# Kernel optimization log

Hardware: AMD Instinct MI355X
Metric: run time of the kernel (lower is better)

## Reference

```python
import jax, jax.numpy as jnp
import numpy as np

B, H, S, D = 2, 12, 2048, 64


def setup_inputs() -> dict:
    key = jax.random.key(0)
    kq, kk, kv = jax.random.split(key, 3)
    q = jax.random.normal(kq, (B, H, S, D), dtype=jnp.float32)
    k = jax.random.normal(kk, (B, H, S, D), dtype=jnp.float32)
    v = jax.random.normal(kv, (B, H, S, D), dtype=jnp.float32)
    # causal mask: True = attend (keep), lower triangle
    mask = jnp.tril(jnp.ones((S, S), dtype=bool))
    return {"q": q, "k": k, "v": v, "mask": mask}


def reference(q, k, v, mask):
    dim = q.shape[-1]
    # [B,H,S,S] scores
    scores = jnp.einsum("bhqd,bhkd->bhqk", q, k) / jnp.sqrt(jnp.asarray(dim, q.dtype))
    # dynamic mask-direction logic from the original module:
    # if the mask is denser in the strict upper triangle, True means "mask out";
    # otherwise True means "keep".
    sq = mask.shape[-1]
    sample = mask.reshape(-1, sq, sq)[0]
    upper = jnp.triu(jnp.ones_like(sample, dtype=bool), k=1)
    flip = jnp.sum(sample & upper) > jnp.sum(sample & ~upper)
    keep = jnp.where(flip, ~mask, mask)  # True = keep
    neg_inf = jnp.asarray(-jnp.inf, scores.dtype)
    scores = jnp.where(keep, scores, neg_inf)
    weights = jax.nn.softmax(scores, axis=-1)
    # dropout with p_drop=0.0 is the identity
    return jnp.einsum("bhqk,bhkd->bhqd", weights, v)
```

## Files before the change

kernel.cpp:

```cpp
#include <hip/hip_runtime.h>
#include <hip/hip_bf16.h>


#define SEQ 2048
#define DH 64
#define NHEADS 24
#define BN 64
#define LDK 72
#define NSLOT (NHEADS * 16 * 4)
#define WS_FA14  ((size_t)NSLOT * 8192 * 2 + (size_t)NSLOT * 128 * 4)

typedef float f32x4 __attribute__((ext_vector_type(4)));
typedef float f32x16 __attribute__((ext_vector_type(16)));
typedef __bf16 bf16x8 __attribute__((ext_vector_type(8)));
typedef __bf16 bf16x4 __attribute__((ext_vector_type(4)));
typedef unsigned int u32;
typedef u32 u32x4 __attribute__((ext_vector_type(4)));
typedef unsigned short u16;

#if __has_builtin(__builtin_amdgcn_exp2f)
#define EXP2F(x) __builtin_amdgcn_exp2f(x)
#else
#define EXP2F(x) exp2f(x)
#endif

#define QSCALE 0.1803368801111204f

static __device__ __forceinline__ u32 pk2(float a, float b) {
    u16 ua = __builtin_bit_cast(u16, (__bf16)a);
    u16 ub = __builtin_bit_cast(u16, (__bf16)b);
    return (u32)ua | ((u32)ub << 16);
}

__global__ __launch_bounds__(256, 3)
void fa23_kernel(const float* __restrict__ q, const float* __restrict__ k,
                 const float* __restrict__ v,
                 __bf16* __restrict__ opart, float* __restrict__ lpart,
                 float* __restrict__ out)
{
    const int bx = blockIdx.x;
    const int xcd = bx & 7;
    const int sub = bx >> 3;
    const int bh = (sub / 40) * 8 + xcd;
    const int rem = 39 - (sub % 40);
    int mt2, st;
    if      (rem >= 36) { mt2 = 15; st = 36; }
    else if (rem >= 32) { mt2 = 14; st = 32; }
    else if (rem >= 28) { mt2 = 13; st = 28; }
    else if (rem >= 24) { mt2 = 12; st = 24; }
    else if (rem >= 21) { mt2 = 11; st = 21; }
    else if (rem >= 18) { mt2 = 10; st = 18; }
    else if (rem >= 15) { mt2 = 9;  st = 15; }
    else if (rem >= 12) { mt2 = 8;  st = 12; }
    else if (rem >= 10) { mt2 = 7;  st = 10; }
    else if (rem >= 8)  { mt2 = 6;  st = 8; }
    else if (rem >= 6)  { mt2 = 5;  st = 6; }
    else if (rem >= 4)  { mt2 = 4;  st = 4; }
    else                { mt2 = rem; st = rem; }
    const int chunk = rem - st;
    const int jt0 = chunk * 8;
    const int jt_end = min(jt0 + 8, 2 * mt2 + 2);
    const int q0 = mt2 * 128;

    const int tid = threadIdx.x;
    const int w = tid >> 6, lane = tid & 63;
    const int l31 = lane & 31;
    const int hb = lane >> 5;

    __shared__ __bf16 Ks[2][4096];
    __shared__ __bf16 Vs[2][4096];

    const float* kh = k + (size_t)bh * SEQ * DH;
    const float* vh = v + (size_t)bh * SEQ * DH;
    const int qg = q0 + w * 32 + l31;

    bf16x8 qn[4];
    {
        const float* qp = q + (size_t)bh * SEQ * DH + (size_t)qg * DH + hb * 8;
        #pragma unroll
        for (int ks = 0; ks < 4; ++ks) {
            f32x4 x0 = *(const f32x4*)(qp + 16 * ks);
            f32x4 x1 = *(const f32x4*)(qp + 16 * ks + 4);
            #pragma unroll
            for (int j = 0; j < 4; ++j) {
                qn[ks][j]     = (__bf16)(x0[j] * QSCALE);
                qn[ks][4 + j] = (__bf16)(x1[j] * QSCALE);
            }
        }
    }

    f32x16 acc_o0 = {}, acc_o1 = {};
    float lsum = 0.0f;

    const int srow0 = tid >> 3;
    const int sg    = tid & 7;
    const int klg   = sg ^ (srow0 & 7);

    const int kb    = (tid & 7) * 4 + ((tid & 128) >> 2);
    const int kb2   = (kb & ~0xC) | ((kb & 4) << 1) | ((kb & 8) >> 1);
    const int dbase = ((tid >> 3) & 15) * 4;

    f32x4 ka[2][2], va[4];
    auto issueKV = [&](int jt) {
        const float* kp = kh + (size_t)(jt * BN + srow0) * DH + klg * 8;
        ka[0][0] = *(const f32x4*)kp;
        ka[0][1] = *(const f32x4*)(kp + 4);
        kp += 32 * DH;
        ka[1][0] = *(const f32x4*)kp;
        ka[1][1] = *(const f32x4*)(kp + 4);
        const float* vpx = vh + (size_t)(jt * BN + kb2) * DH + dbase;
        #pragma unroll
        for (int ii = 0; ii < 4; ++ii) va[ii] = *(const f32x4*)(vpx + ii * DH);
    };
    auto commitKV = [&](int b) {
        #pragma unroll
        for (int s = 0; s < 2; ++s) {
            bf16x8 o;
            #pragma unroll
            for (int jj = 0; jj < 4; ++jj) {
                o[jj]     = (__bf16)ka[s][0][jj];
                o[4 + jj] = (__bf16)ka[s][1][jj];
            }
            *(bf16x8*)((char*)Ks[b] + s * 4096 + tid * 16) = o;
        }
        #pragma unroll
        for (int dd = 0; dd < 4; ++dd) {
            const int d = dbase + dd;
            bf16x4 p4v;
            #pragma unroll
            for (int ii = 0; ii < 4; ++ii) p4v[ii] = (__bf16)va[ii][dd];
            *(bf16x4*)((char*)Vs[b] + d * 128 +
                       ((((kb >> 3) ^ (d & 7)) << 4) | ((kb & 7) * 2))) = p4v;
        }
    };

    issueKV(jt0);
    commitKV(0);
    if (jt0 + 1 < jt_end) issueKV(jt0 + 1);
    __syncthreads();

    int buf = 0;
    for (int jt = jt0; jt < jt_end; ++jt) {
        if (jt + 1 < jt_end) commitKV(buf ^ 1);
        if (jt + 2 < jt_end) issueKV(jt + 2);

        const char* Kb = (const char*)Ks[buf];
        const char* Vb = (const char*)Vs[buf];
        f32x16 sa0 = {}, sa1 = {};
        __builtin_amdgcn_s_setprio(1);
        #pragma unroll
        for (int ks = 0; ks < 4; ++ks) {
            bf16x8 kf0 = *(const bf16x8*)(Kb + l31 * 128 +
                                          (((2 * ks + hb) ^ (lane & 7)) << 4));
            bf16x8 kf1 = *(const bf16x8*)(Kb + (32 + l31) * 128 +
                                          (((2 * ks + hb) ^ (lane & 7)) << 4));
            sa0 = __builtin_amdgcn_mfma_f32_32x32x16_bf16(kf0, qn[ks], sa0, 0, 0, 0);
            sa1 = __builtin_amdgcn_mfma_f32_32x32x16_bf16(kf1, qn[ks], sa1, 0, 0, 0);
        }
        __builtin_amdgcn_s_setprio(0);

        if (jt >= 2 * mt2) {
            #pragma unroll
            for (int reg = 0; reg < 16; ++reg) {
                const int kvr = jt * 64 + (reg & 3) + 8 * (reg >> 2) + 4 * hb;
                if (kvr > qg)      sa0[reg] = -1e30f;
                if (kvr + 32 > qg) sa1[reg] = -1e30f;
            }
        }

        u32 pk[8][2];
        #pragma unroll
        for (int sp = 0; sp < 4; ++sp) {
            float e0 = EXP2F(sa0[4 * sp + 0]), e1 = EXP2F(sa0[4 * sp + 1]);
            float e2 = EXP2F(sa0[4 * sp + 2]), e3 = EXP2F(sa0[4 * sp + 3]);
            float f0 = EXP2F(sa1[4 * sp + 0]), f1 = EXP2F(sa1[4 * sp + 1]);
            float f2 = EXP2F(sa1[4 * sp + 2]), f3 = EXP2F(sa1[4 * sp + 3]);
            lsum += ((e0 + e1) + (e2 + e3)) + ((f0 + f1) + (f2 + f3));
            pk[sp][0]     = pk2(e0, e1); pk[sp][1]     = pk2(e2, e3);
            pk[4 + sp][0] = pk2(f0, f1); pk[4 + sp][1] = pk2(f2, f3);
        }

        __builtin_amdgcn_s_setprio(1);
        #pragma unroll
        for (int s = 0; s < 4; ++s) {
            u32x4 uv;
            uv[0] = pk[2 * s][0];
            uv[1] = pk[2 * s][1];
            uv[2] = pk[2 * s + 1][0];
            uv[3] = pk[2 * s + 1][1];
            bf16x8 pf = __builtin_bit_cast(bf16x8, uv);
            bf16x8 vf0 = *(const bf16x8*)(Vb + l31 * 128 +
                                          (((2 * s + hb) ^ (lane & 7)) << 4));
            bf16x8 vf1 = *(const bf16x8*)(Vb + (32 + l31) * 128 +
                                          (((2 * s + hb) ^ (lane & 7)) << 4));
            acc_o0 = __builtin_amdgcn_mfma_f32_32x32x16_bf16(pf, vf0, acc_o0, 0, 0, 0);
            acc_o1 = __builtin_amdgcn_mfma_f32_32x32x16_bf16(pf, vf1, acc_o1, 0, 0, 0);
        }
        __builtin_amdgcn_s_setprio(0);

        if (jt + 1 < jt_end) __syncthreads();
        buf ^= 1;
    }

    const float ltot = lsum + __shfl_xor(lsum, 32, 64);

    if (2 * mt2 + 2 <= 8) {
        float* oh = out + (size_t)bh * SEQ * DH;
        #pragma unroll
        for (int reg = 0; reg < 16; ++reg) {
            const int rr = (reg & 3) + 8 * (reg >> 2) + 4 * hb;
            const float lr = __shfl(ltot, rr, 64);
            const float inv = 1.0f / lr;
            const int row = q0 + w * 32 + rr;
            oh[(size_t)row * DH + l31]      = acc_o0[reg] * inv;
            oh[(size_t)row * DH + 32 + l31] = acc_o1[reg] * inv;
        }
    } else {
        const int slot = (bh * 16 + mt2) * 4 + chunk;
        __bf16* po = opart + (size_t)slot * 8192;
        #pragma unroll
        for (int reg = 0; reg < 16; ++reg) {
            const int row = w * 32 + (reg & 3) + 8 * (reg >> 2) + 4 * hb;
            po[row * 64 + l31]      = (__bf16)acc_o0[reg];
            po[row * 64 + 32 + l31] = (__bf16)acc_o1[reg];
        }
        if (hb == 0) lpart[(size_t)slot * 128 + w * 32 + l31] = ltot;
    }
}

__global__ __launch_bounds__(256)
void fa_reduce(const __bf16* __restrict__ opart, const float* __restrict__ lpart,
               float* __restrict__ out)
{
    const int bx = blockIdx.x;
    const int xcd = bx & 7;
    const int r2 = bx >> 3;
    const int bh = (r2 / 12) * 8 + xcd;
    const int mt2 = 4 + (r2 % 12);
    const int nc = (mt2 >> 2) + 1;
    const int base = (bh * 16 + mt2) * 4;
    const int tid = threadIdx.x;
    #pragma unroll
    for (int rnd = 0; rnd < 8; ++rnd) {
        const int flat = rnd * 1024 + tid * 4;
        const int row = flat >> 6;
        float o0 = 0, o1 = 0, o2 = 0, o3 = 0, l = 0;
        for (int c = 0; c < nc; ++c) {
            bf16x4 ov = *(const bf16x4*)(opart + (size_t)(base + c) * 8192 + flat);
            o0 += (float)ov[0]; o1 += (float)ov[1]; o2 += (float)ov[2]; o3 += (float)ov[3];
            l += lpart[(size_t)(base + c) * 128 + row];
        }
        const float inv = 1.0f / l;
        f32x4 res = { o0 * inv, o1 * inv, o2 * inv, o3 * inv };
        *(f32x4*)(out + (size_t)bh * SEQ * DH + (size_t)mt2 * 8192 + flat) = res;
    }
}

__global__ __launch_bounds__(256, 2)
void fa_causal_kernel(const float* __restrict__ q, const float* __restrict__ k,
                      const float* __restrict__ v, float* __restrict__ out)
{
    const int mt = 31 - (blockIdx.x & 31);
    const int bh = blockIdx.x >> 5;
    const int tid = threadIdx.x;
    const int w = tid >> 6, lane = tid & 63;
    const int g = lane >> 4, li = lane & 15;
    const int m0 = mt * 64;
    __shared__ __bf16 KsF[BN][LDK];
    __shared__ __bf16 VsF[DH][LDK];
    __shared__ __bf16 PsF[4][16][LDK];
    const size_t head_off = (size_t)bh * SEQ * DH;
    const float* qh = q + head_off;
    const float* kh = k + head_off;
    const float* vh = v + head_off;
    float* oh = out + head_off;
    const int qrow = m0 + w * 16 + li;
    bf16x8 qf[2];
    {
        const float* qp = qh + (size_t)qrow * DH + g * 8;
        #pragma unroll
        for (int c = 0; c < 2; ++c) {
            const float* p = qp + c * 32;
            #pragma unroll
            for (int jj = 0; jj < 8; ++jj) qf[c][jj] = (__bf16)p[jj];
        }
    }
    f32x4 acc[4] = {};
    float mrow[4], lrow[4];
    #pragma unroll
    for (int r = 0; r < 4; ++r) { mrow[r] = -1e30f; lrow[r] = 0.0f; }
    const float scale = 0.125f;
    const int srow = tid >> 2, scol = (tid & 3) * 16;
    for (int jt = 0; jt <= mt; ++jt) {
        const int kv0 = jt * BN;
        __syncthreads();
        {
            const float* kp = kh + (size_t)(kv0 + srow) * DH + scol;
            __bf16 tmp[16];
            #pragma unroll
            for (int jj = 0; jj < 16; ++jj) tmp[jj] = (__bf16)kp[jj];
            *(bf16x8*)&KsF[srow][scol]     = *(bf16x8*)&tmp[0];
            *(bf16x8*)&KsF[srow][scol + 8] = *(bf16x8*)&tmp[8];
            const float* vp = vh + (size_t)(kv0 + srow) * DH + scol;
            #pragma unroll
            for (int jj = 0; jj < 16; ++jj) VsF[scol + jj][srow] = (__bf16)vp[jj];
        }
        __syncthreads();
        float s4[4][4];
        #pragma unroll
        for (int t = 0; t < 4; ++t) {
            f32x4 sa = {};
            #pragma unroll
            for (int c = 0; c < 2; ++c) {
                bf16x8 kfr = *(const bf16x8*)&KsF[t * 16 + li][c * 32 + g * 8];
                sa = __builtin_amdgcn_mfma_f32_16x16x32_bf16(qf[c], kfr, sa, 0, 0, 0);
            }
            #pragma unroll
            for (int r = 0; r < 4; ++r) s4[t][r] = sa[r] * scale;
        }
        if (jt == mt) {
            #pragma unroll
            for (int t = 0; t < 4; ++t) {
                const int col = kv0 + t * 16 + li;
                #pragma unroll
                for (int r = 0; r < 4; ++r)
                    if (col > m0 + w * 16 + g * 4 + r) s4[t][r] = -1e30f;
            }
        }
        #pragma unroll
        for (int r = 0; r < 4; ++r) {
            float mx = fmaxf(fmaxf(s4[0][r], s4[1][r]), fmaxf(s4[2][r], s4[3][r]));
            #pragma unroll
            for (int off = 1; off < 16; off <<= 1)
                mx = fmaxf(mx, __shfl_xor(mx, off, 64));
            const float mnew = fmaxf(mrow[r], mx);
            const float alpha = __expf(mrow[r] - mnew);
            mrow[r] = mnew;
            float ps = 0.0f;
            #pragma unroll
            for (int t = 0; t < 4; ++t) {
                const float p = __expf(s4[t][r] - mnew);
                s4[t][r] = p;
                ps += p;
            }
            #pragma unroll
            for (int off = 1; off < 16; off <<= 1)
                ps += __shfl_xor(ps, off, 64);
            lrow[r] = lrow[r] * alpha + ps;
            #pragma unroll
            for (int t = 0; t < 4; ++t) acc[t][r] *= alpha;
        }
        #pragma unroll
        for (int t = 0; t < 4; ++t)
            #pragma unroll
            for (int r = 0; r < 4; ++r)
                PsF[w][g * 4 + r][t * 16 + li] = (__bf16)s4[t][r];
        __syncthreads();
        #pragma unroll
        for (int c = 0; c < 2; ++c) {
            bf16x8 pf = *(const bf16x8*)&PsF[w][li][c * 32 + g * 8];
            #pragma unroll
            for (int t = 0; t < 4; ++t) {
                bf16x8 vfr = *(const bf16x8*)&VsF[t * 16 + li][c * 32 + g * 8];
                acc[t] = __builtin_amdgcn_mfma_f32_16x16x32_bf16(pf, vfr, acc[t], 0, 0, 0);
            }
        }
    }
    #pragma unroll
    for (int r = 0; r < 4; ++r) {
        const int row = m0 + w * 16 + g * 4 + r;
        const float inv = 1.0f / lrow[r];
        float* op = oh + (size_t)row * DH + li;
        #pragma unroll
        for (int t = 0; t < 4; ++t) op[t * 16] = acc[t][r] * inv;
    }
}

extern "C" void kernel_launch(void* const* d_in, const int* in_sizes, int n_in,
                              void* d_out, int out_size, void* d_ws, size_t ws_size,
                              hipStream_t stream) {
    (void)in_sizes; (void)n_in; (void)out_size;
    const float* q = (const float*)d_in[0];
    const float* k = (const float*)d_in[1];
    const float* v = (const float*)d_in[2];
    float* out = (float*)d_out;

    if (ws_size >= WS_FA14) {
        __bf16* opart = (__bf16*)d_ws;
        float* lpart = (float*)((char*)d_ws + (size_t)NSLOT * 8192 * 2);
        fa23_kernel<<<dim3(960), dim3(256), 0, stream>>>(q, k, v, opart, lpart, out);
        fa_reduce<<<dim3(288), dim3(256), 0, stream>>>(opart, lpart, out);
    } else {
        fa_causal_kernel<<<dim3(NHEADS * 32), dim3(256), 0, stream>>>(q, k, v, out);
    }
}
```

Before: 130.7 us.

## Pre-convert K/V to bf16 (V transposed) and stage tiles via global_load_lds

Adds a prep kernel that converts K to bf16 and writes V as a transposed, permuted bf16 copy in the workspace. The attention kernel then loads K/V tiles straight into LDS with global_load_lds, dropping the register staging, per-tile conversion and scatter writes, and moving from a two-deep register prefetch to a single-ahead LDS double buffer. Launch bounds rise to 4 waves per SIMD. In exchange it adds a third kernel launch plus an extra pass over K/V in global memory, and needs more workspace.

```diff
diff --git a/kernel.cpp b/kernel.cpp
--- a/kernel.cpp
+++ b/kernel.cpp
@@ -7,8 +7,10 @@
 #define NHEADS 24
 #define BN 64
 #define LDK 72
+#define ELEMS_PER_TENSOR (NHEADS * SEQ * DH)
 #define NSLOT (NHEADS * 16 * 4)
-#define WS_FA14  ((size_t)NSLOT * 8192 * 2 + (size_t)NSLOT * 128 * 4)
+#define WS_KV    ((size_t)2 * ELEMS_PER_TENSOR * 2)
+#define WS_FA11  (WS_KV + (size_t)NSLOT * 8192 * 2 + (size_t)NSLOT * 128 * 4)
 
 typedef float f32x4 __attribute__((ext_vector_type(4)));
 typedef float f32x16 __attribute__((ext_vector_type(16)));
@@ -26,15 +28,60 @@
 
 #define QSCALE 0.1803368801111204f
 
+#define GLOAD_LDS16(g, l)                                                     \
+    __builtin_amdgcn_global_load_lds(                                         \
+        (const __attribute__((address_space(1))) void*)(g),                   \
+        (__attribute__((address_space(3))) void*)(l), 16, 0, 0)
+
 static __device__ __forceinline__ u32 pk2(float a, float b) {
     u16 ua = __builtin_bit_cast(u16, (__bf16)a);
     u16 ub = __builtin_bit_cast(u16, (__bf16)b);
     return (u32)ua | ((u32)ub << 16);
 }
 
-__global__ __launch_bounds__(256, 3)
-void fa23_kernel(const float* __restrict__ q, const float* __restrict__ k,
-                 const float* __restrict__ v,
+__global__ __launch_bounds__(256)
+void prep_kernel(const float* __restrict__ k, const float* __restrict__ v,
+                 __bf16* __restrict__ ks, __bf16* __restrict__ vt)
+{
+    __shared__ __bf16 T[64][LDK];
+    const int bx = blockIdx.x;
+    const int tid = threadIdx.x;
+    if (bx < 1536) {
+        const int idx = (bx * 256 + tid) * 8;
+        f32x4 a = *(const f32x4*)(k + idx);
+        f32x4 b = *(const f32x4*)(k + idx + 4);
+        bf16x8 o;
+        #pragma unroll
+        for (int j = 0; j < 4; ++j) { o[j] = (__bf16)a[j]; o[4 + j] = (__bf16)b[j]; }
+        *(bf16x8*)(ks + idx) = o;
+    } else {
+        const int b2 = bx - 1536;
+        const int bh = b2 >> 5;
+        const int s0 = (b2 & 31) * 64;
+        const int r = tid >> 2, c0 = (tid & 3) * 16;
+        const float* vp = v + (size_t)bh * SEQ * DH + (size_t)(s0 + r) * DH + c0;
+        __bf16 tmp[16];
+        #pragma unroll
+        for (int jj = 0; jj < 16; ++jj) tmp[jj] = (__bf16)vp[jj];
+        *(bf16x8*)&T[r][c0]     = *(bf16x8*)&tmp[0];
+        *(bf16x8*)&T[r][c0 + 8] = *(bf16x8*)&tmp[8];
+        __syncthreads();
+        const int d = tid >> 2, j0 = (tid & 3) * 16;
+        __bf16 o[16];
+        #pragma unroll
+        for (int jj = 0; jj < 16; ++jj) {
+            const int js = (jj & 3) | ((jj & 4) << 1) | ((jj & 8) >> 1);
+            o[jj] = T[j0 + js][d];
+        }
+        __bf16* op = vt + (size_t)bh * DH * SEQ + (size_t)d * SEQ + s0 + j0;
+        *(bf16x8*)op       = *(bf16x8*)&o[0];
+        *(bf16x8*)(op + 8) = *(bf16x8*)&o[8];
+    }
+}
+
+__global__ __launch_bounds__(256, 4)
+void fa24_kernel(const float* __restrict__ q, const __bf16* __restrict__ ks,
+                 const __bf16* __restrict__ vt,
                  __bf16* __restrict__ opart, float* __restrict__ lpart,
                  float* __restrict__ out)
 {
@@ -70,21 +117,21 @@
     __shared__ __bf16 Ks[2][4096];
     __shared__ __bf16 Vs[2][4096];
 
-    const float* kh = k + (size_t)bh * SEQ * DH;
-    const float* vh = v + (size_t)bh * SEQ * DH;
+    const __bf16* khb = ks + (size_t)bh * SEQ * DH;
+    const __bf16* vhb = vt + (size_t)bh * DH * SEQ;
     const int qg = q0 + w * 32 + l31;
 
     bf16x8 qn[4];
     {
         const float* qp = q + (size_t)bh * SEQ * DH + (size_t)qg * DH + hb * 8;
         #pragma unroll
-        for (int ks = 0; ks < 4; ++ks) {
-            f32x4 x0 = *(const f32x4*)(qp + 16 * ks);
-            f32x4 x1 = *(const f32x4*)(qp + 16 * ks + 4);
+        for (int kq = 0; kq < 4; ++kq) {
+            f32x4 x0 = *(const f32x4*)(qp + 16 * kq);
+            f32x4 x1 = *(const f32x4*)(qp + 16 * kq + 4);
             #pragma unroll
             for (int j = 0; j < 4; ++j) {
-                qn[ks][j]     = (__bf16)(x0[j] * QSCALE);
-                qn[ks][4 + j] = (__bf16)(x1[j] * QSCALE);
+                qn[kq][j]     = (__bf16)(x0[j] * QSCALE);
+                qn[kq][4 + j] = (__bf16)(x1[j] * QSCALE);
             }
         }
     }
@@ -92,70 +139,41 @@
     f32x16 acc_o0 = {}, acc_o1 = {};
     float lsum = 0.0f;
 
-    const int srow0 = tid >> 3;
-    const int sg    = tid & 7;
-    const int klg   = sg ^ (srow0 & 7);
-
-    const int kb    = (tid & 7) * 4 + ((tid & 128) >> 2);
-    const int kb2   = (kb & ~0xC) | ((kb & 4) << 1) | ((kb & 8) >> 1);
-    const int dbase = ((tid >> 3) & 15) * 4;
-
-    f32x4 ka[2][2], va[4];
-    auto issueKV = [&](int jt) {
-        const float* kp = kh + (size_t)(jt * BN + srow0) * DH + klg * 8;
-        ka[0][0] = *(const f32x4*)kp;
-        ka[0][1] = *(const f32x4*)(kp + 4);
-        kp += 32 * DH;
-        ka[1][0] = *(const f32x4*)kp;
-        ka[1][1] = *(const f32x4*)(kp + 4);
-        const float* vpx = vh + (size_t)(jt * BN + kb2) * DH + dbase;
-        #pragma unroll
-        for (int ii = 0; ii < 4; ++ii) va[ii] = *(const f32x4*)(vpx + ii * DH);
+    const int krow = tid >> 3;
+    const int kcg  = (tid & 7) ^ ((tid >> 3) & 7);
+    const int vd0  = tid >> 3;
+    const int vkg  = (tid & 7) ^ ((tid >> 3) & 7);
+
+    auto stage = [&](int jt, int b) {
+        GLOAD_LDS16(khb + (size_t)(jt * BN + krow) * DH + kcg * 8,
+                    (char*)Ks[b] + tid * 16);
+        GLOAD_LDS16(khb + (size_t)(jt * BN + 32 + krow) * DH + kcg * 8,
+                    (char*)Ks[b] + 4096 + tid * 16);
+        GLOAD_LDS16(vhb + (size_t)vd0 * SEQ + jt * BN + vkg * 8,
+                    (char*)Vs[b] + tid * 16);
+        GLOAD_LDS16(vhb + (size_t)(32 + vd0) * SEQ + jt * BN + vkg * 8,
+                    (char*)Vs[b] + 4096 + tid * 16);
     };
-    auto commitKV = [&](int b) {
-        #pragma unroll
-        for (int s = 0; s < 2; ++s) {
-            bf16x8 o;
-            #pragma unroll
-            for (int jj = 0; jj < 4; ++jj) {
-                o[jj]     = (__bf16)ka[s][0][jj];
-                o[4 + jj] = (__bf16)ka[s][1][jj];
-            }
-            *(bf16x8*)((char*)Ks[b] + s * 4096 + tid * 16) = o;
-        }
-        #pragma unroll
-        for (int dd = 0; dd < 4; ++dd) {
-            const int d = dbase + dd;
-            bf16x4 p4v;
-            #pragma unroll
-            for (int ii = 0; ii < 4; ++ii) p4v[ii] = (__bf16)va[ii][dd];
-            *(bf16x4*)((char*)Vs[b] + d * 128 +
-                       ((((kb >> 3) ^ (d & 7)) << 4) | ((kb & 7) * 2))) = p4v;
-        }
-    };
-
-    issueKV(jt0);
-    commitKV(0);
-    if (jt0 + 1 < jt_end) issueKV(jt0 + 1);
+
+    stage(jt0, 0);
     __syncthreads();
 
     int buf = 0;
     for (int jt = jt0; jt < jt_end; ++jt) {
-        if (jt + 1 < jt_end) commitKV(buf ^ 1);
-        if (jt + 2 < jt_end) issueKV(jt + 2);
+        if (jt + 1 < jt_end) stage(jt + 1, buf ^ 1);
 
         const char* Kb = (const char*)Ks[buf];
         const char* Vb = (const char*)Vs[buf];
         f32x16 sa0 = {}, sa1 = {};
         __builtin_amdgcn_s_setprio(1);
         #pragma unroll
-        for (int ks = 0; ks < 4; ++ks) {
+        for (int kq = 0; kq < 4; ++kq) {
             bf16x8 kf0 = *(const bf16x8*)(Kb + l31 * 128 +
-                                          (((2 * ks + hb) ^ (lane & 7)) << 4));
+                                          (((2 * kq + hb) ^ (lane & 7)) << 4));
             bf16x8 kf1 = *(const bf16x8*)(Kb + (32 + l31) * 128 +
-                                          (((2 * ks + hb) ^ (lane & 7)) << 4));
-            sa0 = __builtin_amdgcn_mfma_f32_32x32x16_bf16(kf0, qn[ks], sa0, 0, 0, 0);
-            sa1 = __builtin_amdgcn_mfma_f32_32x32x16_bf16(kf1, qn[ks], sa1, 0, 0, 0);
+                                          (((2 * kq + hb) ^ (lane & 7)) << 4));
+            sa0 = __builtin_amdgcn_mfma_f32_32x32x16_bf16(kf0, qn[kq], sa0, 0, 0, 0);
+            sa1 = __builtin_amdgcn_mfma_f32_32x32x16_bf16(kf1, qn[kq], sa1, 0, 0, 0);
         }
         __builtin_amdgcn_s_setprio(0);
 
@@ -385,10 +403,13 @@
     const float* v = (const float*)d_in[2];
     float* out = (float*)d_out;
 
-    if (ws_size >= WS_FA14) {
-        __bf16* opart = (__bf16*)d_ws;
-        float* lpart = (float*)((char*)d_ws + (size_t)NSLOT * 8192 * 2);
-        fa23_kernel<<<dim3(960), dim3(256), 0, stream>>>(q, k, v, opart, lpart, out);
+    if (ws_size >= WS_FA11) {
+        __bf16* ks = (__bf16*)d_ws;
+        __bf16* vt = ks + ELEMS_PER_TENSOR;
+        __bf16* opart = (__bf16*)((char*)d_ws + WS_KV);
+        float* lpart = (float*)((char*)d_ws + WS_KV + (size_t)NSLOT * 8192 * 2);
+        prep_kernel<<<dim3(1536 + 768), dim3(256), 0, stream>>>(k, v, ks, vt);
+        fa24_kernel<<<dim3(960), dim3(256), 0, stream>>>(q, ks, vt, opart, lpart, out);
         fa_reduce<<<dim3(288), dim3(256), 0, stream>>>(opart, lpart, out);
     } else {
         fa_causal_kernel<<<dim3(NHEADS * 32), dim3(256), 0, stream>>>(q, k, v, out);
```

New measurement: 128.2 us. No clear change (-1.9%).
